# Performance work log

Measured on AMD Instinct MI355X. Metric: run time of the kernel, lower is better.

The kernel has to match this reference:

```python
import jax, jax.numpy as jnp
import numpy as np

N = 50000      # nodes
E = 800000     # edges (avg degree 16)
D_IN = 64
D_H = 64


def setup_inputs() -> dict:
    key = jax.random.key(0)
    k = jax.random.split(key, 4)
    x = jax.random.normal(k[0], (N, D_IN), dtype=jnp.float32)
    edge_index = jax.random.randint(k[1], (2, E), 0, N, dtype=jnp.int64)
    W1 = jax.random.normal(k[2], (D_IN, D_H), dtype=jnp.float32) * (1.0 / np.sqrt(D_IN))
    b1 = jnp.zeros((D_H,), dtype=jnp.float32)
    W2 = jax.random.normal(k[3], (D_H, 1), dtype=jnp.float32) * (1.0 / np.sqrt(D_H))
    b2 = jnp.zeros((1,), dtype=jnp.float32)
    return {"x": x, "edge_index": edge_index, "W1": W1, "b1": b1, "W2": W2, "b2": b2}


def gcn_conv(x, src, dst, W, b):
    """PyG-style GCNConv: linear -> symmetric-normalized scatter-aggregate + bias.
    src/dst already include self-loops."""
    n = x.shape[0]
    h = x @ W                                                   # [N, Dout]
    deg = jax.ops.segment_sum(jnp.ones_like(dst, dtype=h.dtype), dst, num_segments=n)
    dinv_sqrt = jnp.where(deg > 0, jax.lax.rsqrt(jnp.maximum(deg, 1e-12)), 0.0)
    norm = dinv_sqrt[src] * dinv_sqrt[dst]                       # [E+N]
    agg = jax.ops.segment_sum(h[src] * norm[:, None], dst, num_segments=n)
    return agg + b


def reference(x, edge_index, W1, b1, W2, b2):
    n = x.shape[0]
    loops = jnp.arange(n, dtype=edge_index.dtype)
    src = jnp.concatenate([edge_index[0], loops])                # add self-loops
    dst = jnp.concatenate([edge_index[1], loops])
    h = jax.nn.relu(gcn_conv(x, src, dst, W1, b1))               # [N, D_H]
    out = gcn_conv(h, src, dst, W2, b2)                          # [N, 1]
    return out.squeeze(-1)                                       # [N]
```

## Files before the change

kernel.cpp:

```cpp
#include <hip/hip_runtime.h>
#include <hip/hip_fp16.h>

#define D 64
#define PW2 128
#define PSH2 7
#define EPB 2048

__global__ __launch_bounds__(512) void k_hist(const int* __restrict__ dst, int E,
                                              int* __restrict__ counts, int NP) {
    extern __shared__ int lh[];
    int t = threadIdx.x, b = blockIdx.x;
    for (int i = t; i < NP; i += 512) lh[i] = 0;
    __syncthreads();
    int base = b * EPB;
#pragma unroll
    for (int k = 0; k < EPB / 512; ++k) {
        int e = base + k * 512 + t;
        if (e < E) atomicAdd(&lh[dst[e] >> PSH2], 1);
    }
    __syncthreads();
    for (int i = t; i < NP; i += 512) counts[(size_t)b * NP + i] = lh[i];
}

__global__ __launch_bounds__(512) void k_scanA(int* __restrict__ counts, int NB, int NP,
                                               int* __restrict__ bin_total) {
    __shared__ int sh[512];
    int t = threadIdx.x, bin = blockIdx.x;
    int v = (t < NB) ? counts[(size_t)t * NP + bin] : 0;
    sh[t] = v;
    __syncthreads();
    for (int off = 1; off < 512; off <<= 1) {
        int u = (t >= off) ? sh[t - off] : 0;
        __syncthreads();
        sh[t] += u;
        __syncthreads();
    }
    if (t < NB) counts[(size_t)t * NP + bin] = sh[t] - v;
    if (t == 511) bin_total[bin] = sh[511];
}

__global__ __launch_bounds__(1024) void k_scanB(const int* __restrict__ bin_total, int NP,
                                                int* __restrict__ bin_base) {
    __shared__ int sh[1024];
    int t = threadIdx.x;
    int i0 = 2 * t, i1 = 2 * t + 1;
    int v0 = (i0 < NP) ? bin_total[i0] : 0;
    int v1 = (i1 < NP) ? bin_total[i1] : 0;
    int s = v0 + v1;
    sh[t] = s;
    __syncthreads();
    for (int off = 1; off < 1024; off <<= 1) {
        int u = (t >= off) ? sh[t - off] : 0;
        __syncthreads();
        sh[t] += u;
        __syncthreads();
    }
    int excl = sh[t] - s;
    if (i0 < NP) bin_base[i0] = excl;
    if (i1 < NP) bin_base[i1] = excl + v0;
    if (t == 1023) bin_base[NP] = sh[1023];
}

__global__ __launch_bounds__(512) void k_scatter(const int* __restrict__ src,
        const int* __restrict__ dst, int E, const int* __restrict__ counts,
        const int* __restrict__ bin_base, int NP, int* __restrict__ csr_e) {
    extern __shared__ int cur[];
    int t = threadIdx.x, b = blockIdx.x;
    for (int i = t; i < NP; i += 512)
        cur[i] = counts[(size_t)b * NP + i] + bin_base[i];
    __syncthreads();
    int base = b * EPB;
#pragma unroll
    for (int k = 0; k < EPB / 512; ++k) {
        int e = base + k * 512 + t;
        if (e < E) {
            int s = src[e], d = dst[e];
            int pos = atomicAdd(&cur[d >> PSH2], 1);
            csr_e[pos] = s | ((d & (PW2 - 1)) << 16);
        }
    }
}

__global__ __launch_bounds__(512) void k_sort2(const int* __restrict__ csr_e,
        const int* __restrict__ bin_base, int n,
        const float4* __restrict__ x4, __half2* __restrict__ xh2,
        int* __restrict__ csr_src, int* __restrict__ row_ptr,
        float* __restrict__ dinv) {
    __shared__ int cnt[PW2];
    __shared__ int sh[512];
    __shared__ int cursor[PW2];
    __shared__ float ldv[PW2];
    int t = threadIdx.x, p = blockIdx.x;
    int beg = bin_base[p], end = bin_base[p + 1];
    if (t < PW2) cnt[t] = 0;
    __syncthreads();
    for (int i = beg + t; i < end; i += 512) atomicAdd(&cnt[csr_e[i] >> 16], 1);
    __syncthreads();
    int val = (t < PW2) ? cnt[t] : 0;
    sh[t] = val;
    __syncthreads();
    for (int off = 1; off < 512; off <<= 1) {
        int u = (t >= off) ? sh[t - off] : 0;
        __syncthreads();
        sh[t] += u;
        __syncthreads();
    }
    int excl = sh[t] - val;
    if (t < PW2) {
        cursor[t] = beg + excl;
        int node = p * PW2 + t;
        float dv = rsqrtf((float)(val + 1));
        ldv[t] = dv;
        if (node <= n) {
            row_ptr[node] = beg + excl;
            if (node < n) dinv[node] = dv;
        }
    }
    __syncthreads();
    for (int i = beg + t; i < end; i += 512) {
        int e = csr_e[i];
        int q = atomicAdd(&cursor[e >> 16], 1);
        csr_src[q] = e & 0xFFFF;
    }
    for (int i = t; i < PW2 * 16; i += 512) {
        int row = i >> 4;
        int node = p * PW2 + row;
        if (node < n) {
            int gi = node * 16 + (i & 15);
            float4 v = x4[gi];
            float s = ldv[row];
            xh2[2 * gi]     = __floats2half2_rn(v.x * s, v.y * s);
            xh2[2 * gi + 1] = __floats2half2_rn(v.z * s, v.w * s);
        }
    }
}

__global__ __launch_bounds__(256) void k_gather(
        const __half2* __restrict__ xh, const float* __restrict__ dinv,
        const int* __restrict__ row_ptr, const int* __restrict__ csr_src,
        float* __restrict__ agg, int n) {
    int tid = threadIdx.x;
    int wave = tid >> 6, lane = tid & 63;
    int eg = lane >> 3, dg = lane & 7;
    int v = blockIdx.x * 4 + wave;
    if (v >= n) return;
    float dv = dinv[v];
    int beg = row_ptr[v], end = row_ptr[v + 1];

    float4 A = make_float4(0.f, 0.f, 0.f, 0.f);
    float4 B = make_float4(0.f, 0.f, 0.f, 0.f);
    float2 f;
#define ACC16(r)                                                        \
    {   __half2 h0 = *(__half2*)&(r).x, h1 = *(__half2*)&(r).y,         \
                h2 = *(__half2*)&(r).z, h3 = *(__half2*)&(r).w;         \
        f = __half22float2(h0); A.x += f.x; A.y += f.y;                 \
        f = __half22float2(h1); A.z += f.x; A.w += f.y;                 \
        f = __half22float2(h2); B.x += f.x; B.y += f.y;                 \
        f = __half22float2(h3); B.z += f.x; B.w += f.y; }

    if (eg == 0) {
        int4 r = *(const int4*)(xh + (size_t)v * 32 + dg * 4);
        ACC16(r);
    }
    int base = beg;
    for (; base + 16 <= end; base += 16) {
        int u0 = csr_src[base + eg];
        int u1 = csr_src[base + 8 + eg];
        int4 r0 = *(const int4*)(xh + (size_t)u0 * 32 + dg * 4);
        int4 r1 = *(const int4*)(xh + (size_t)u1 * 32 + dg * 4);
        ACC16(r0);
        ACC16(r1);
    }
    for (; base < end; base += 8) {
        int idx = base + eg;
        if (idx < end) {
            int u = csr_src[idx];
            int4 r = *(const int4*)(xh + (size_t)u * 32 + dg * 4);
            ACC16(r);
        }
    }
#undef ACC16
#pragma unroll
    for (int off = 8; off <= 32; off <<= 1) {
        A.x += __shfl_xor(A.x, off, 64); A.y += __shfl_xor(A.y, off, 64);
        A.z += __shfl_xor(A.z, off, 64); A.w += __shfl_xor(A.w, off, 64);
        B.x += __shfl_xor(B.x, off, 64); B.y += __shfl_xor(B.y, off, 64);
        B.z += __shfl_xor(B.z, off, 64); B.w += __shfl_xor(B.w, off, 64);
    }
    if (eg == 0) {
        A.x *= dv; A.y *= dv; A.z *= dv; A.w *= dv;
        B.x *= dv; B.y *= dv; B.z *= dv; B.w *= dv;
        *(float4*)&agg[(size_t)v * D + dg * 8] = A;
        *(float4*)&agg[(size_t)v * D + dg * 8 + 4] = B;
    }
}

#define NPW 16
__global__ __launch_bounds__(256) void k_gemm(
        const float* __restrict__ agg, const float* __restrict__ dinv,
        const float* __restrict__ W1, const float* __restrict__ b1,
        const float* __restrict__ W2, float* __restrict__ sd, int n) {
    __shared__ float lrow[4][D];
    int tid = threadIdx.x;
    int wave = tid >> 6, lane = tid & 63;
    float w1c[D];
#pragma unroll
    for (int d = 0; d < D; ++d) w1c[d] = W1[d * D + lane];
    float b1l = b1[lane], w2l = W2[lane];
    int v0 = (blockIdx.x * 4 + wave) * NPW;
    for (int k = 0; k < NPW; ++k) {
        int v = v0 + k;
        if (v >= n) break;
        lrow[wave][lane] = agg[(size_t)v * D + lane];
        __builtin_amdgcn_wave_barrier();
        float h = b1l;
#pragma unroll
        for (int db = 0; db < D; db += 4) {
            float4 r = *(const float4*)&lrow[wave][db];
            h = fmaf(r.x, w1c[db], h);
            h = fmaf(r.y, w1c[db + 1], h);
            h = fmaf(r.z, w1c[db + 2], h);
            h = fmaf(r.w, w1c[db + 3], h);
        }
        float tt = fmaxf(h, 0.0f) * w2l;
#pragma unroll
        for (int off = 1; off <= 32; off <<= 1) tt += __shfl_xor(tt, off, 64);
        if (lane == 0) sd[v] = tt * dinv[v];
        __builtin_amdgcn_wave_barrier();
    }
}

__global__ __launch_bounds__(256) void k_out(const float* __restrict__ sd,
        const float* __restrict__ dinv, const int* __restrict__ row_ptr,
        const int* __restrict__ csr_src, const float* __restrict__ b2,
        float* __restrict__ out, int n) {
    int t = blockIdx.x * blockDim.x + threadIdx.x;
    int v = t >> 3, r = t & 7;
    if (v >= n) return;
    int beg = row_ptr[v], end = row_ptr[v + 1];
    float a = (r == 0) ? sd[v] : 0.0f;
    for (int i = beg + r; i < end; i += 8) a += sd[csr_src[i]];
    a += __shfl_xor(a, 1, 64);
    a += __shfl_xor(a, 2, 64);
    a += __shfl_xor(a, 4, 64);
    if (r == 0) out[v] = b2[0] + a * dinv[v];
}

extern "C" void kernel_launch(void* const* d_in, const int* in_sizes, int n_in,
                              void* d_out, int out_size, void* d_ws, size_t ws_size,
                              hipStream_t stream) {
    const float* x  = (const float*)d_in[0];
    const int*   ei = (const int*)d_in[1];
    const float* W1 = (const float*)d_in[2];
    const float* b1 = (const float*)d_in[3];
    const float* W2 = (const float*)d_in[4];
    const float* b2 = (const float*)d_in[5];

    int n = in_sizes[0] / D;
    int E = in_sizes[1] / 2;
    const int* src = ei;
    const int* dst = ei + E;

    int NP = (n + PW2 - 1) / PW2;
    int NB = (E + EPB - 1) / EPB;

    char* ws = (char*)d_ws;
    auto take = [&](size_t bytes) {
        char* p = ws;
        ws += (bytes + 255) & ~(size_t)255;
        return p;
    };
    int*     counts    = (int*)take((size_t)NB * NP * sizeof(int));
    int*     bin_total = (int*)take((size_t)NP * sizeof(int));
    int*     bin_base  = (int*)take((size_t)(NP + 1) * sizeof(int));
    int*     csr_e     = (int*)take((size_t)E * sizeof(int));
    int*     csr_src   = (int*)take((size_t)E * sizeof(int));
    int*     row_ptr   = (int*)take((size_t)(n + 1) * sizeof(int));
    float*   dinv      = (float*)take((size_t)n * sizeof(float));
    float*   sd        = (float*)take((size_t)n * sizeof(float));
    float*   agg       = (float*)take((size_t)n * D * sizeof(float));
    __half2* xh        = (__half2*)take((size_t)n * D * sizeof(__half));

    float* out = (float*)d_out;
    size_t ldsNP = (size_t)NP * sizeof(int);

    k_hist<<<NB, 512, ldsNP, stream>>>(dst, E, counts, NP);
    k_scanA<<<NP, 512, 0, stream>>>(counts, NB, NP, bin_total);
    k_scanB<<<1, 1024, 0, stream>>>(bin_total, NP, bin_base);
    k_scatter<<<NB, 512, ldsNP, stream>>>(src, dst, E, counts, bin_base, NP, csr_e);
    k_sort2<<<NP, 512, 0, stream>>>(csr_e, bin_base, n, (const float4*)x, xh,
                                    csr_src, row_ptr, dinv);

    k_gather<<<(n + 3) / 4, 256, 0, stream>>>(xh, dinv, row_ptr, csr_src, agg, n);
    k_gemm<<<(n + 4 * NPW - 1) / (4 * NPW), 256, 0, stream>>>(agg, dinv, W1, b1,
                                                              W2, sd, n);
    k_out<<<((size_t)n * 8 + 255) / 256, 256, 0, stream>>>(sd, dinv, row_ptr, csr_src,
                                                           b2, out, n);
}
```

Baseline: 83.99 us.

## Fuse CSR-building kernels into one cooperative kernel with grid syncs

Merges the histogram, two scan stages, scatter and per-bin sort kernels into a single cooperative launch that uses grid-wide barriers between phases. Every block redundantly computes the bin-base scan in shared memory, so the separate single-block scan kernel and its global array go away. The aim is to remove four kernel launch gaps and their tail drain. In exchange the grid is limited to what can be co-resident (391 blocks of 512 threads), and each grid.sync adds barrier latency.

Result: slower. 238.7 us (+184.2%).

```diff
diff --git a/kernel.cpp b/kernel.cpp
--- a/kernel.cpp
+++ b/kernel.cpp
@@ -1,136 +1,134 @@
 #include <hip/hip_runtime.h>
 #include <hip/hip_fp16.h>
+#include <hip/hip_cooperative_groups.h>
+
+namespace cg = cooperative_groups;
 
 #define D 64
 #define PW2 128
 #define PSH2 7
 #define EPB 2048
 
-__global__ __launch_bounds__(512) void k_hist(const int* __restrict__ dst, int E,
-                                              int* __restrict__ counts, int NP) {
-    extern __shared__ int lh[];
-    int t = threadIdx.x, b = blockIdx.x;
-    for (int i = t; i < NP; i += 512) lh[i] = 0;
-    __syncthreads();
-    int base = b * EPB;
-#pragma unroll
-    for (int k = 0; k < EPB / 512; ++k) {
-        int e = base + k * 512 + t;
-        if (e < E) atomicAdd(&lh[dst[e] >> PSH2], 1);
-    }
-    __syncthreads();
-    for (int i = t; i < NP; i += 512) counts[(size_t)b * NP + i] = lh[i];
-}
-
-__global__ __launch_bounds__(512) void k_scanA(int* __restrict__ counts, int NB, int NP,
-                                               int* __restrict__ bin_total) {
-    __shared__ int sh[512];
-    int t = threadIdx.x, bin = blockIdx.x;
-    int v = (t < NB) ? counts[(size_t)t * NP + bin] : 0;
-    sh[t] = v;
-    __syncthreads();
-    for (int off = 1; off < 512; off <<= 1) {
-        int u = (t >= off) ? sh[t - off] : 0;
-        __syncthreads();
-        sh[t] += u;
-        __syncthreads();
-    }
-    if (t < NB) counts[(size_t)t * NP + bin] = sh[t] - v;
-    if (t == 511) bin_total[bin] = sh[511];
-}
-
-__global__ __launch_bounds__(1024) void k_scanB(const int* __restrict__ bin_total, int NP,
-                                                int* __restrict__ bin_base) {
-    __shared__ int sh[1024];
-    int t = threadIdx.x;
-    int i0 = 2 * t, i1 = 2 * t + 1;
-    int v0 = (i0 < NP) ? bin_total[i0] : 0;
-    int v1 = (i1 < NP) ? bin_total[i1] : 0;
-    int s = v0 + v1;
-    sh[t] = s;
-    __syncthreads();
-    for (int off = 1; off < 1024; off <<= 1) {
-        int u = (t >= off) ? sh[t - off] : 0;
-        __syncthreads();
-        sh[t] += u;
-        __syncthreads();
-    }
-    int excl = sh[t] - s;
-    if (i0 < NP) bin_base[i0] = excl;
-    if (i1 < NP) bin_base[i1] = excl + v0;
-    if (t == 1023) bin_base[NP] = sh[1023];
-}
-
-__global__ __launch_bounds__(512) void k_scatter(const int* __restrict__ src,
-        const int* __restrict__ dst, int E, const int* __restrict__ counts,
-        const int* __restrict__ bin_base, int NP, int* __restrict__ csr_e) {
-    extern __shared__ int cur[];
-    int t = threadIdx.x, b = blockIdx.x;
-    for (int i = t; i < NP; i += 512)
-        cur[i] = counts[(size_t)b * NP + i] + bin_base[i];
-    __syncthreads();
-    int base = b * EPB;
-#pragma unroll
-    for (int k = 0; k < EPB / 512; ++k) {
-        int e = base + k * 512 + t;
-        if (e < E) {
-            int s = src[e], d = dst[e];
-            int pos = atomicAdd(&cur[d >> PSH2], 1);
-            csr_e[pos] = s | ((d & (PW2 - 1)) << 16);
-        }
-    }
-}
-
-__global__ __launch_bounds__(512) void k_sort2(const int* __restrict__ csr_e,
-        const int* __restrict__ bin_base, int n,
+__global__ __launch_bounds__(512) void k_front(
+        const int* __restrict__ src, const int* __restrict__ dst, int E, int n,
+        int NB, int NP,
+        int* __restrict__ counts, int* __restrict__ bin_total,
+        int* __restrict__ csr_e,
         const float4* __restrict__ x4, __half2* __restrict__ xh2,
         int* __restrict__ csr_src, int* __restrict__ row_ptr,
         float* __restrict__ dinv) {
+    __shared__ int lh[512];
+    __shared__ int sh[512];
+    __shared__ int bb[513];
     __shared__ int cnt[PW2];
-    __shared__ int sh[512];
     __shared__ int cursor[PW2];
     __shared__ float ldv[PW2];
-    int t = threadIdx.x, p = blockIdx.x;
-    int beg = bin_base[p], end = bin_base[p + 1];
-    if (t < PW2) cnt[t] = 0;
-    __syncthreads();
-    for (int i = beg + t; i < end; i += 512) atomicAdd(&cnt[csr_e[i] >> 16], 1);
-    __syncthreads();
-    int val = (t < PW2) ? cnt[t] : 0;
-    sh[t] = val;
-    __syncthreads();
-    for (int off = 1; off < 512; off <<= 1) {
-        int u = (t >= off) ? sh[t - off] : 0;
-        __syncthreads();
-        sh[t] += u;
-        __syncthreads();
-    }
-    int excl = sh[t] - val;
-    if (t < PW2) {
-        cursor[t] = beg + excl;
-        int node = p * PW2 + t;
-        float dv = rsqrtf((float)(val + 1));
-        ldv[t] = dv;
-        if (node <= n) {
-            row_ptr[node] = beg + excl;
-            if (node < n) dinv[node] = dv;
-        }
-    }
-    __syncthreads();
-    for (int i = beg + t; i < end; i += 512) {
-        int e = csr_e[i];
-        int q = atomicAdd(&cursor[e >> 16], 1);
-        csr_src[q] = e & 0xFFFF;
-    }
-    for (int i = t; i < PW2 * 16; i += 512) {
-        int row = i >> 4;
-        int node = p * PW2 + row;
-        if (node < n) {
-            int gi = node * 16 + (i & 15);
-            float4 v = x4[gi];
-            float s = ldv[row];
-            xh2[2 * gi]     = __floats2half2_rn(v.x * s, v.y * s);
-            xh2[2 * gi + 1] = __floats2half2_rn(v.z * s, v.w * s);
+    cg::grid_group grid = cg::this_grid();
+    int t = threadIdx.x, b = blockIdx.x;
+
+    if (b < NB) {
+        for (int i = t; i < NP; i += 512) lh[i] = 0;
+        __syncthreads();
+        int base = b * EPB;
+#pragma unroll
+        for (int k = 0; k < EPB / 512; ++k) {
+            int e = base + k * 512 + t;
+            if (e < E) atomicAdd(&lh[dst[e] >> PSH2], 1);
+        }
+        __syncthreads();
+        for (int i = t; i < NP; i += 512) counts[(size_t)b * NP + i] = lh[i];
+    }
+    grid.sync();
+
+    if (b < NP) {
+        int v = (t < NB) ? counts[(size_t)t * NP + b] : 0;
+        sh[t] = v;
+        __syncthreads();
+        for (int off = 1; off < 512; off <<= 1) {
+            int u = (t >= off) ? sh[t - off] : 0;
+            __syncthreads();
+            sh[t] += u;
+            __syncthreads();
+        }
+        if (t < NB) counts[(size_t)t * NP + b] = sh[t] - v;
+        if (t == 511) bin_total[b] = sh[511];
+    }
+    grid.sync();
+
+    {
+        int v = (t < NP) ? bin_total[t] : 0;
+        sh[t] = v;
+        __syncthreads();
+        for (int off = 1; off < 512; off <<= 1) {
+            int u = (t >= off) ? sh[t - off] : 0;
+            __syncthreads();
+            sh[t] += u;
+            __syncthreads();
+        }
+        if (t < NP) bb[t] = sh[t] - v;
+        if (t == NP - 1) bb[NP] = sh[t];
+        __syncthreads();
+    }
+
+    if (b < NB) {
+        for (int i = t; i < NP; i += 512)
+            lh[i] = counts[(size_t)b * NP + i] + bb[i];
+        __syncthreads();
+        int base = b * EPB;
+#pragma unroll
+        for (int k = 0; k < EPB / 512; ++k) {
+            int e = base + k * 512 + t;
+            if (e < E) {
+                int s = src[e], d = dst[e];
+                int pos = atomicAdd(&lh[d >> PSH2], 1);
+                csr_e[pos] = s | ((d & (PW2 - 1)) << 16);
+            }
+        }
+    }
+    grid.sync();
+
+    if (b < NP) {
+        int beg = bb[b], end = bb[b + 1];
+        if (t < PW2) cnt[t] = 0;
+        __syncthreads();
+        for (int i = beg + t; i < end; i += 512) atomicAdd(&cnt[csr_e[i] >> 16], 1);
+        __syncthreads();
+        int val = (t < PW2) ? cnt[t] : 0;
+        sh[t] = val;
+        __syncthreads();
+        for (int off = 1; off < 512; off <<= 1) {
+            int u = (t >= off) ? sh[t - off] : 0;
+            __syncthreads();
+            sh[t] += u;
+            __syncthreads();
+        }
+        int excl = sh[t] - val;
+        if (t < PW2) {
+            cursor[t] = beg + excl;
+            int node = b * PW2 + t;
+            float dv = rsqrtf((float)(val + 1));
+            ldv[t] = dv;
+            if (node <= n) {
+                row_ptr[node] = beg + excl;
+                if (node < n) dinv[node] = dv;
+            }
+        }
+        __syncthreads();
+        for (int i = beg + t; i < end; i += 512) {
+            int e = csr_e[i];
+            int q = atomicAdd(&cursor[e >> 16], 1);
+            csr_src[q] = e & 0xFFFF;
+        }
+        for (int i = t; i < PW2 * 16; i += 512) {
+            int row = i >> 4;
+            int node = b * PW2 + row;
+            if (node < n) {
+                int gi = node * 16 + (i & 15);
+                float4 v = x4[gi];
+                float s = ldv[row];
+                xh2[2 * gi]     = __floats2half2_rn(v.x * s, v.y * s);
+                xh2[2 * gi + 1] = __floats2half2_rn(v.z * s, v.w * s);
+            }
         }
     }
 }
@@ -263,6 +261,7 @@
 
     int NP = (n + PW2 - 1) / PW2;
     int NB = (E + EPB - 1) / EPB;
+    int G  = (NB > NP) ? NB : NP;
 
     char* ws = (char*)d_ws;
     auto take = [&](size_t bytes) {
@@ -272,7 +271,6 @@
     };
     int*     counts    = (int*)take((size_t)NB * NP * sizeof(int));
     int*     bin_total = (int*)take((size_t)NP * sizeof(int));
-    int*     bin_base  = (int*)take((size_t)(NP + 1) * sizeof(int));
     int*     csr_e     = (int*)take((size_t)E * sizeof(int));
     int*     csr_src   = (int*)take((size_t)E * sizeof(int));
     int*     row_ptr   = (int*)take((size_t)(n + 1) * sizeof(int));
@@ -282,14 +280,16 @@
     __half2* xh        = (__half2*)take((size_t)n * D * sizeof(__half));
 
     float* out = (float*)d_out;
-    size_t ldsNP = (size_t)NP * sizeof(int);
-
-    k_hist<<<NB, 512, ldsNP, stream>>>(dst, E, counts, NP);
-    k_scanA<<<NP, 512, 0, stream>>>(counts, NB, NP, bin_total);
-    k_scanB<<<1, 1024, 0, stream>>>(bin_total, NP, bin_base);
-    k_scatter<<<NB, 512, ldsNP, stream>>>(src, dst, E, counts, bin_base, NP, csr_e);
-    k_sort2<<<NP, 512, 0, stream>>>(csr_e, bin_base, n, (const float4*)x, xh,
-                                    csr_src, row_ptr, dinv);
+
+    const float4* x4c = (const float4*)x;
+    void* args[] = {
+        (void*)&src, (void*)&dst, (void*)&E, (void*)&n,
+        (void*)&NB, (void*)&NP,
+        (void*)&counts, (void*)&bin_total, (void*)&csr_e,
+        (void*)&x4c, (void*)&xh,
+        (void*)&csr_src, (void*)&row_ptr, (void*)&dinv
+    };
+    hipLaunchCooperativeKernel((void*)k_front, dim3(G), dim3(512), args, 0, stream);
 
     k_gather<<<(n + 3) / 4, 256, 0, stream>>>(xh, dinv, row_ptr, csr_src, agg, n);
     k_gemm<<<(n + 4 * NPW - 1) / (4 * NPW), 256, 0, stream>>>(agg, dinv, W1, b1,
```

## Apply W1 before aggregation and fuse bias/ReLU/W2 into gather epilogue

Applied to the files above, without the earlier changes.

Reorders the first layer so that x@W1 is computed per node (scaled by dinv, stored in fp16) before neighbor aggregation, rather than aggregating x and multiplying afterwards. With that order the gather kernel can apply bias, ReLU and the W2 dot product directly in its epilogue, so the fp32 agg buffer write/read and the separate GEMM pass over it disappear. The dense GEMM pass now reads x instead of agg, and the x-to-fp16 conversion moves out of the sort kernel.

Result: faster. 81.29 us (-3.2%).

```diff
diff --git a/kernel.cpp b/kernel.cpp
--- a/kernel.cpp
+++ b/kernel.cpp
@@ -83,13 +83,11 @@
 
 __global__ __launch_bounds__(512) void k_sort2(const int* __restrict__ csr_e,
         const int* __restrict__ bin_base, int n,
-        const float4* __restrict__ x4, __half2* __restrict__ xh2,
         int* __restrict__ csr_src, int* __restrict__ row_ptr,
         float* __restrict__ dinv) {
     __shared__ int cnt[PW2];
     __shared__ int sh[512];
     __shared__ int cursor[PW2];
-    __shared__ float ldv[PW2];
     int t = threadIdx.x, p = blockIdx.x;
     int beg = bin_base[p], end = bin_base[p + 1];
     if (t < PW2) cnt[t] = 0;
@@ -109,11 +107,9 @@
     if (t < PW2) {
         cursor[t] = beg + excl;
         int node = p * PW2 + t;
-        float dv = rsqrtf((float)(val + 1));
-        ldv[t] = dv;
         if (node <= n) {
             row_ptr[node] = beg + excl;
-            if (node < n) dinv[node] = dv;
+            if (node < n) dinv[node] = rsqrtf((float)(val + 1));
         }
     }
     __syncthreads();
@@ -122,23 +118,43 @@
         int q = atomicAdd(&cursor[e >> 16], 1);
         csr_src[q] = e & 0xFFFF;
     }
-    for (int i = t; i < PW2 * 16; i += 512) {
-        int row = i >> 4;
-        int node = p * PW2 + row;
-        if (node < n) {
-            int gi = node * 16 + (i & 15);
-            float4 v = x4[gi];
-            float s = ldv[row];
-            xh2[2 * gi]     = __floats2half2_rn(v.x * s, v.y * s);
-            xh2[2 * gi + 1] = __floats2half2_rn(v.z * s, v.w * s);
-        }
+}
+
+#define NPW 16
+__global__ __launch_bounds__(256) void k_zw(
+        const float* __restrict__ x, const float* __restrict__ dinv,
+        const float* __restrict__ W1, __half* __restrict__ zh, int n) {
+    __shared__ float lrow[4][D];
+    int tid = threadIdx.x;
+    int wave = tid >> 6, lane = tid & 63;
+    float w1c[D];
+#pragma unroll
+    for (int d = 0; d < D; ++d) w1c[d] = W1[d * D + lane];
+    int v0 = (blockIdx.x * 4 + wave) * NPW;
+    for (int k = 0; k < NPW; ++k) {
+        int v = v0 + k;
+        if (v >= n) break;
+        lrow[wave][lane] = x[(size_t)v * D + lane];
+        __builtin_amdgcn_wave_barrier();
+        float h = 0.0f;
+#pragma unroll
+        for (int db = 0; db < D; db += 4) {
+            float4 r = *(const float4*)&lrow[wave][db];
+            h = fmaf(r.x, w1c[db], h);
+            h = fmaf(r.y, w1c[db + 1], h);
+            h = fmaf(r.z, w1c[db + 2], h);
+            h = fmaf(r.w, w1c[db + 3], h);
+        }
+        zh[(size_t)v * D + lane] = __float2half(h * dinv[v]);
+        __builtin_amdgcn_wave_barrier();
     }
 }
 
 __global__ __launch_bounds__(256) void k_gather(
-        const __half2* __restrict__ xh, const float* __restrict__ dinv,
+        const __half2* __restrict__ zh, const float* __restrict__ dinv,
         const int* __restrict__ row_ptr, const int* __restrict__ csr_src,
-        float* __restrict__ agg, int n) {
+        const float* __restrict__ b1, const float* __restrict__ W2,
+        float* __restrict__ sd, int n) {
     int tid = threadIdx.x;
     int wave = tid >> 6, lane = tid & 63;
     int eg = lane >> 3, dg = lane & 7;
@@ -159,15 +175,15 @@
         f = __half22float2(h3); B.z += f.x; B.w += f.y; }
 
     if (eg == 0) {
-        int4 r = *(const int4*)(xh + (size_t)v * 32 + dg * 4);
+        int4 r = *(const int4*)(zh + (size_t)v * 32 + dg * 4);
         ACC16(r);
     }
     int base = beg;
     for (; base + 16 <= end; base += 16) {
         int u0 = csr_src[base + eg];
         int u1 = csr_src[base + 8 + eg];
-        int4 r0 = *(const int4*)(xh + (size_t)u0 * 32 + dg * 4);
-        int4 r1 = *(const int4*)(xh + (size_t)u1 * 32 + dg * 4);
+        int4 r0 = *(const int4*)(zh + (size_t)u0 * 32 + dg * 4);
+        int4 r1 = *(const int4*)(zh + (size_t)u1 * 32 + dg * 4);
         ACC16(r0);
         ACC16(r1);
     }
@@ -175,7 +191,7 @@
         int idx = base + eg;
         if (idx < end) {
             int u = csr_src[idx];
-            int4 r = *(const int4*)(xh + (size_t)u * 32 + dg * 4);
+            int4 r = *(const int4*)(zh + (size_t)u * 32 + dg * 4);
             ACC16(r);
         }
     }
@@ -187,47 +203,23 @@
         B.x += __shfl_xor(B.x, off, 64); B.y += __shfl_xor(B.y, off, 64);
         B.z += __shfl_xor(B.z, off, 64); B.w += __shfl_xor(B.w, off, 64);
     }
-    if (eg == 0) {
-        A.x *= dv; A.y *= dv; A.z *= dv; A.w *= dv;
-        B.x *= dv; B.y *= dv; B.z *= dv; B.w *= dv;
-        *(float4*)&agg[(size_t)v * D + dg * 8] = A;
-        *(float4*)&agg[(size_t)v * D + dg * 8 + 4] = B;
-    }
-}
-
-#define NPW 16
-__global__ __launch_bounds__(256) void k_gemm(
-        const float* __restrict__ agg, const float* __restrict__ dinv,
-        const float* __restrict__ W1, const float* __restrict__ b1,
-        const float* __restrict__ W2, float* __restrict__ sd, int n) {
-    __shared__ float lrow[4][D];
-    int tid = threadIdx.x;
-    int wave = tid >> 6, lane = tid & 63;
-    float w1c[D];
-#pragma unroll
-    for (int d = 0; d < D; ++d) w1c[d] = W1[d * D + lane];
-    float b1l = b1[lane], w2l = W2[lane];
-    int v0 = (blockIdx.x * 4 + wave) * NPW;
-    for (int k = 0; k < NPW; ++k) {
-        int v = v0 + k;
-        if (v >= n) break;
-        lrow[wave][lane] = agg[(size_t)v * D + lane];
-        __builtin_amdgcn_wave_barrier();
-        float h = b1l;
-#pragma unroll
-        for (int db = 0; db < D; db += 4) {
-            float4 r = *(const float4*)&lrow[wave][db];
-            h = fmaf(r.x, w1c[db], h);
-            h = fmaf(r.y, w1c[db + 1], h);
-            h = fmaf(r.z, w1c[db + 2], h);
-            h = fmaf(r.w, w1c[db + 3], h);
-        }
-        float tt = fmaxf(h, 0.0f) * w2l;
-#pragma unroll
-        for (int off = 1; off <= 32; off <<= 1) tt += __shfl_xor(tt, off, 64);
-        if (lane == 0) sd[v] = tt * dinv[v];
-        __builtin_amdgcn_wave_barrier();
-    }
+    float4 b1a = *(const float4*)&b1[dg * 8];
+    float4 b1b = *(const float4*)&b1[dg * 8 + 4];
+    float4 w2a = *(const float4*)&W2[dg * 8];
+    float4 w2b = *(const float4*)&W2[dg * 8 + 4];
+    float part;
+    part  = fmaxf(fmaf(dv, A.x, b1a.x), 0.f) * w2a.x;
+    part += fmaxf(fmaf(dv, A.y, b1a.y), 0.f) * w2a.y;
+    part += fmaxf(fmaf(dv, A.z, b1a.z), 0.f) * w2a.z;
+    part += fmaxf(fmaf(dv, A.w, b1a.w), 0.f) * w2a.w;
+    part += fmaxf(fmaf(dv, B.x, b1b.x), 0.f) * w2b.x;
+    part += fmaxf(fmaf(dv, B.y, b1b.y), 0.f) * w2b.y;
+    part += fmaxf(fmaf(dv, B.z, b1b.z), 0.f) * w2b.z;
+    part += fmaxf(fmaf(dv, B.w, b1b.w), 0.f) * w2b.w;
+    part += __shfl_xor(part, 1, 64);
+    part += __shfl_xor(part, 2, 64);
+    part += __shfl_xor(part, 4, 64);
+    if (lane == 0) sd[v] = part * dv;
 }
 
 __global__ __launch_bounds__(256) void k_out(const float* __restrict__ sd,
@@ -278,8 +270,7 @@
     int*     row_ptr   = (int*)take((size_t)(n + 1) * sizeof(int));
     float*   dinv      = (float*)take((size_t)n * sizeof(float));
     float*   sd        = (float*)take((size_t)n * sizeof(float));
-    float*   agg       = (float*)take((size_t)n * D * sizeof(float));
-    __half2* xh        = (__half2*)take((size_t)n * D * sizeof(__half));
+    __half*  zh        = (__half*)take((size_t)n * D * sizeof(__half));
 
     float* out = (float*)d_out;
     size_t ldsNP = (size_t)NP * sizeof(int);
@@ -288,12 +279,12 @@
     k_scanA<<<NP, 512, 0, stream>>>(counts, NB, NP, bin_total);
     k_scanB<<<1, 1024, 0, stream>>>(bin_total, NP, bin_base);
     k_scatter<<<NB, 512, ldsNP, stream>>>(src, dst, E, counts, bin_base, NP, csr_e);
-    k_sort2<<<NP, 512, 0, stream>>>(csr_e, bin_base, n, (const float4*)x, xh,
-                                    csr_src, row_ptr, dinv);
-
-    k_gather<<<(n + 3) / 4, 256, 0, stream>>>(xh, dinv, row_ptr, csr_src, agg, n);
-    k_gemm<<<(n + 4 * NPW - 1) / (4 * NPW), 256, 0, stream>>>(agg, dinv, W1, b1,
-                                                              W2, sd, n);
+    k_sort2<<<NP, 512, 0, stream>>>(csr_e, bin_base, n, csr_src, row_ptr, dinv);
+
+    k_zw<<<(n + 4 * NPW - 1) / (4 * NPW), 256, 0, stream>>>(x, dinv, W1, zh, n);
+
+    k_gather<<<(n + 3) / 4, 256, 0, stream>>>((const __half2*)zh, dinv, row_ptr,
+                                              csr_src, b1, W2, sd, n);
     k_out<<<((size_t)n * 8 + 255) / 256, 256, 0, stream>>>(sd, dinv, row_ptr, csr_src,
                                                            b2, out, n);
 }
```
